# Optimization experiments

Measured on AMD Instinct MI355X. Metric: run time of the kernel, lower is better.

The kernel has to match this reference:

```python
import jax, jax.numpy as jnp
import numpy as np

B, N, NS, D, H = 32, 4096, 16, 512, 8
DH = D // H          # dims_per_head = 64
DFF = 4 * D          # ff_mlp hidden
SCALE = DH ** -0.5
EPS = 1e-8           # slot-attention renorm eps
LN_EPS = 1e-5        # torch LayerNorm default
ITERS = 3


def layer_norm(x, g, b):
    mu = jnp.mean(x, axis=-1, keepdims=True)
    var = jnp.mean((x - mu) ** 2, axis=-1, keepdims=True)
    return (x - mu) * jax.lax.rsqrt(var + LN_EPS) * g + b


def setup_inputs() -> dict:
    key = jax.random.key(0)
    ks = jax.random.split(key, 8)
    s = 0.02
    return {
        "inputs": jax.random.normal(ks[0], (B, N, D), jnp.float32),
        "conditioning": jax.random.normal(ks[1], (B, NS, D), jnp.float32),
        # norm_input
        "ln_in_g": jnp.ones((D,), jnp.float32),
        "ln_in_b": jnp.zeros((D,), jnp.float32),
        # projections (no bias: use_projection_bias=False)
        "Wk": jax.random.normal(ks[2], (D, D), jnp.float32) * s,
        "Wv": jax.random.normal(ks[3], (D, D), jnp.float32) * s,
        "Wq": jax.random.normal(ks[4], (D, D), jnp.float32) * s,
        "Wo": jax.random.normal(ks[5], (D, D), jnp.float32) * s,
        # norm_slots / norm_slots_ff_mlp
        "ln_s_g": jnp.ones((D,), jnp.float32),
        "ln_s_b": jnp.zeros((D,), jnp.float32),
        "ln_f_g": jnp.ones((D,), jnp.float32),
        "ln_f_b": jnp.zeros((D,), jnp.float32),
        # ff_mlp: Linear(D,4D) -> ReLU -> Linear(4D,D)
        "W1": jax.random.normal(ks[6], (D, DFF), jnp.float32) * s,
        "b1": jnp.zeros((DFF,), jnp.float32),
        "W2": jax.random.normal(ks[7], (DFF, D), jnp.float32) * s,
        "b2": jnp.zeros((D,), jnp.float32),
    }


def reference(inputs, conditioning, ln_in_g, ln_in_b, Wk, Wv, Wq, Wo,
              ln_s_g, ln_s_b, ln_f_g, ln_f_b, W1, b1, W2, b2):
    b = inputs.shape[0]
    x = layer_norm(inputs, ln_in_g, ln_in_b)                 # [b, n, D]
    k = (x @ Wk.T).reshape(b, N, H, DH)                      # [b, n, h, dh]
    v = (x @ Wv.T).reshape(b, N, H, DH)

    slots = conditioning
    attn_mean = None
    for _ in range(ITERS):
        slots_prev = slots
        s = layer_norm(slots, ln_s_g, ln_s_b)
        q = (s @ Wq.T).reshape(b, NS, H, DH)                 # [b, ns, h, dh]
        dots = jnp.einsum("bihd,bjhd->bihj", q, k) * SCALE   # [b, ns, h, n]
        # softmax over flattened (slots, heads) axis, per input location j
        attn = jax.nn.softmax(dots.reshape(b, NS * H, N), axis=1)
        attn = attn.reshape(b, NS, H, N)
        attn_before = attn
        attn = attn + EPS
        attn = attn / jnp.sum(attn, axis=-1, keepdims=True)  # renorm over j
        updates = jnp.einsum("bjhd,bihj->bihd", v, attn)     # [b, ns, h, dh]
        updates = updates.reshape(b, NS, D)
        slots = updates @ Wo.T + slots_prev                  # to_o + residual
        slots_prev_ff = slots
        s2 = layer_norm(slots, ln_f_g, ln_f_b)
        s2 = jax.nn.relu(s2 @ W1 + b1) @ W2 + b2             # ff_mlp
        slots = s2 + slots_prev_ff
        attn_mean = jnp.mean(attn_before, axis=2)            # [b, ns, n]
    return slots, attn_mean
```

## Files before the change

### kernel.cpp

```cpp
#include <hip/hip_runtime.h>
#include <cstdint>
#include <cstddef>

typedef __attribute__((ext_vector_type(8))) short short8;
typedef __attribute__((ext_vector_type(4))) short short4v;
typedef __attribute__((ext_vector_type(8))) __bf16 bf16x8;
typedef __attribute__((ext_vector_type(4))) float f32x4;
typedef unsigned short u16;

static constexpr int Bb = 32, Nn = 4096, NSs = 16, Dd = 512, Hh = 8, DFF = 2048;
static constexpr float SCALE = 0.125f;
static constexpr float EPSR  = 1e-8f;
static constexpr float LN_EPS = 1e-5f;

__device__ __forceinline__ u16 f2b(float x) {
  union { float f; uint32_t u; } a; a.f = x;
  uint32_t r = a.u + 0x7fffu + ((a.u >> 16) & 1u);
  return (u16)(r >> 16);
}

__device__ __forceinline__ f32x4 mfma16(short8 a, short8 b, f32x4 c) {
  return __builtin_amdgcn_mfma_f32_16x16x32_bf16(
      __builtin_bit_cast(bf16x8, a), __builtin_bit_cast(bf16x8, b), c, 0, 0, 0);
}

__device__ __forceinline__ void gload16(const u16* g, u16* l) {
  __builtin_amdgcn_global_load_lds(
      (const __attribute__((address_space(1))) void*)g,
      (__attribute__((address_space(3))) void*)l, 16, 0, 0);
}


__global__ __launch_bounds__(256) void ln_rows(const float* __restrict__ src,
    const float* __restrict__ g, const float* __restrict__ bt,
    u16* __restrict__ dst, int R) {
  int row = blockIdx.x * 4 + (threadIdx.x >> 6);
  if (row >= R) return;
  int lane = threadIdx.x & 63;
  const float* p = src + (size_t)row * Dd + lane * 8;
  float4 u0 = *(const float4*)p;
  float4 u1 = *(const float4*)(p + 4);
  float x[8] = {u0.x,u0.y,u0.z,u0.w,u1.x,u1.y,u1.z,u1.w};
  float s = 0.f, s2 = 0.f;
#pragma unroll
  for (int e = 0; e < 8; ++e) { s += x[e]; s2 += x[e]*x[e]; }
#pragma unroll
  for (int m = 1; m < 64; m <<= 1) { s += __shfl_xor(s, m); s2 += __shfl_xor(s2, m); }
  float mean = s * (1.f/512.f);
  float var  = s2 * (1.f/512.f) - mean*mean;
  float rstd = rsqrtf(var + LN_EPS);
  union { u16 o[8]; short8 v; } ou;
#pragma unroll
  for (int e = 0; e < 8; ++e)
    ou.o[e] = f2b((x[e]-mean)*rstd*g[lane*8+e] + bt[lane*8+e]);
  *(short8*)(dst + (size_t)row * Dd + lane * 8) = ou.v;
}

__global__ __launch_bounds__(256, 2) void gemm_kv(const u16* __restrict__ A,
    const u16* __restrict__ Bk, const u16* __restrict__ Bv,
    u16* __restrict__ Ck, u16* __restrict__ CvT) {
  __shared__ u16 lA[2][128*32];
  __shared__ u16 lK[2][128*32];
  __shared__ u16 lV[2][128*32];
  const int tid = threadIdx.x, lane = tid & 63, wid = tid >> 6;
  const int wr = wid >> 1, wc = wid & 1;
  const int n  = blockIdx.y * 4 + blockIdx.x;
  const int orig = (n & 7) * 512 + (n >> 3);
  const int bm = (orig >> 2) * 128, bn = (orig & 3) * 128;
  const size_t BN = (size_t)Bb * Nn;
  f32x4 ak[4][4] = {};
  f32x4 av[4][4] = {};
  const int srow = wid*16 + (lane >> 2);
  const int scol = ((lane & 3) ^ ((lane >> 3) & 3)) * 8;
  const u16* Ap = A  + (size_t)(bm + srow) * Dd + scol;
  const u16* Kp = Bk + (size_t)(bn + srow) * Dd + scol;
  const u16* Vp = Bv + (size_t)(bn + srow) * Dd + scol;
  const int ldb = wid * 512;
  const int li = lane & 15, lk = lane >> 4;
  const int csw = (lk ^ ((li >> 1) & 3)) * 8;
  gload16(Ap, &lA[0][ldb]);
  gload16(Ap + (size_t)64*Dd, &lA[0][ldb + 2048]);
  gload16(Kp, &lK[0][ldb]);
  gload16(Kp + (size_t)64*Dd, &lK[0][ldb + 2048]);
  gload16(Vp, &lV[0][ldb]);
  gload16(Vp + (size_t)64*Dd, &lV[0][ldb + 2048]);
  int cur = 0;
  for (int t = 0; t < 16; ++t) {
    __syncthreads();
    const int nx = cur ^ 1;
    if (t < 15) {
      const int k0 = (t + 1) * 32;
      gload16(Ap + k0, &lA[nx][ldb]);
      gload16(Ap + (size_t)64*Dd + k0, &lA[nx][ldb + 2048]);
      gload16(Kp + k0, &lK[nx][ldb]);
      gload16(Kp + (size_t)64*Dd + k0, &lK[nx][ldb + 2048]);
      gload16(Vp + k0, &lV[nx][ldb]);
      gload16(Vp + (size_t)64*Dd + k0, &lV[nx][ldb + 2048]);
    }
    short8 af[4], kf[4], vf[4];
#pragma unroll
    for (int m = 0; m < 4; ++m)
      af[m] = *(const short8*)&lA[cur][(wr*64 + m*16 + li)*32 + csw];
#pragma unroll
    for (int nn2 = 0; nn2 < 4; ++nn2) {
      kf[nn2] = *(const short8*)&lK[cur][(wc*64 + nn2*16 + li)*32 + csw];
      vf[nn2] = *(const short8*)&lV[cur][(wc*64 + nn2*16 + li)*32 + csw];
    }
#pragma unroll
    for (int m = 0; m < 4; ++m)
#pragma unroll
      for (int nn2 = 0; nn2 < 4; ++nn2) {
        ak[m][nn2] = mfma16(af[m], kf[nn2], ak[m][nn2]);
        av[m][nn2] = mfma16(af[m], vf[nn2], av[m][nn2]);
      }
    cur = nx;
  }
  const int lr = lk * 4;
#pragma unroll
  for (int m = 0; m < 4; ++m)
#pragma unroll
    for (int nn2 = 0; nn2 < 4; ++nn2) {
      int row = bm + wr*64 + m*16 + lr;
      int col = bn + wc*64 + nn2*16 + li;
      f32x4 vk = ak[m][nn2];
#pragma unroll
      for (int r = 0; r < 4; ++r)
        Ck[(size_t)(row + r) * Dd + col] = f2b(vk[r]);
      f32x4 vv = av[m][nn2];
      union { u16 o[4]; short4v v4; } ou;
#pragma unroll
      for (int r = 0; r < 4; ++r) ou.o[r] = f2b(vv[r]);
      *(short4v*)&CvT[(size_t)col * BN + row] = ou.v4;
    }
}

template<int EP>
__global__ __launch_bounds__(256) void gemm64(const u16* __restrict__ A,
    const u16* __restrict__ Bw, void* __restrict__ Cp,
    const float* __restrict__ bias, const float* __restrict__ res,
    int N, int K) {
  __shared__ u16 lA[2][64*32];
  __shared__ u16 lB[2][64*32];
  const int tid = threadIdx.x, lane = tid & 63, wid = tid >> 6;
  const int wr = wid >> 1, wc = wid & 1;
  const int bm = blockIdx.y * 64, bn = blockIdx.x * 64;
  f32x4 acc[2][2] = {};
  const int srow = wid*16 + (lane >> 2);
  const int scol = ((lane & 3) ^ ((lane >> 3) & 3)) * 8;
  const u16* Ap = A + (size_t)(bm + srow) * K + scol;
  const u16* Bp = Bw + (size_t)(bn + srow) * K + scol;
  const int ldb = wid * 512;
  const int li = lane & 15, lk = lane >> 4;
  const int csw = (lk ^ ((li >> 1) & 3)) * 8;
  const int nsteps = K >> 5;
  gload16(Ap, &lA[0][ldb]);
  gload16(Bp, &lB[0][ldb]);
  int cur = 0;
  for (int t = 0; t < nsteps; ++t) {
    __syncthreads();
    const int nx = cur ^ 1;
    if (t + 1 < nsteps) {
      const int k0 = (t + 1) * 32;
      gload16(Ap + k0, &lA[nx][ldb]);
      gload16(Bp + k0, &lB[nx][ldb]);
    }
    short8 af[2], bf[2];
#pragma unroll
    for (int m = 0; m < 2; ++m)
      af[m] = *(const short8*)&lA[cur][(wr*32 + m*16 + li)*32 + csw];
#pragma unroll
    for (int nn2 = 0; nn2 < 2; ++nn2)
      bf[nn2] = *(const short8*)&lB[cur][(wc*32 + nn2*16 + li)*32 + csw];
#pragma unroll
    for (int m = 0; m < 2; ++m)
#pragma unroll
      for (int nn2 = 0; nn2 < 2; ++nn2)
        acc[m][nn2] = mfma16(af[m], bf[nn2], acc[m][nn2]);
    cur = nx;
  }
  const int lr = lk * 4;
#pragma unroll
  for (int m = 0; m < 2; ++m)
#pragma unroll
    for (int nn2 = 0; nn2 < 2; ++nn2) {
      int row = bm + wr*32 + m*16 + lr;
      int col = bn + wc*32 + nn2*16 + li;
      f32x4 v = acc[m][nn2];
#pragma unroll
      for (int r = 0; r < 4; ++r) {
        size_t off = (size_t)(row + r) * N + col;
        float x = v[r];
        if constexpr (EP == 0) ((u16*)Cp)[off] = f2b(x);
        else if constexpr (EP == 1) ((float*)Cp)[off] = x + res[off];
        else if constexpr (EP == 2) { x += bias[col]; ((u16*)Cp)[off] = f2b(x > 0.f ? x : 0.f); }
        else ((float*)Cp)[off] = x + bias[col] + res[off];
      }
    }
}

__global__ __launch_bounds__(256) void attn_a(const u16* __restrict__ q,
    const u16* __restrict__ kk, u16* __restrict__ attnb,
    float* __restrict__ rowsum, float* __restrict__ attn_mean) {
  const int jt = blockIdx.x, b = blockIdx.y;
  const int tid = threadIdx.x, lane = tid & 63, wid = tid >> 6;
  __shared__ float sc[64][129];
  __shared__ float red[4][64];
  const int li = lane & 15, lk = lane >> 4;
#pragma unroll
  for (int hh = 0; hh < 2; ++hh) {
    const int h = wid * 2 + hh;
    const u16* qb = q + (((size_t)b*16 + li)*8 + h)*64 + lk*8;
    short8 a0 = *(const short8*)qb;
    short8 a1 = *(const short8*)(qb + 32);
#pragma unroll
    for (int n = 0; n < 4; ++n) {
      const u16* kb = kk + ((size_t)b*Nn + jt*64 + n*16 + li)*Dd + h*64 + lk*8;
      f32x4 acc = {};
      acc = mfma16(a0, *(const short8*)kb, acc);
      acc = mfma16(a1, *(const short8*)(kb + 32), acc);
#pragma unroll
      for (int r = 0; r < 4; ++r)
        sc[n*16 + li][(lk*4 + r)*8 + h] = acc[r] * SCALE;
    }
  }
  __syncthreads();
  const int jl = tid & 63, qt = tid >> 6;
  float mx = -1e30f;
#pragma unroll
  for (int e = 0; e < 32; ++e) mx = fmaxf(mx, sc[jl][qt*32 + e]);
  red[qt][jl] = mx;
  __syncthreads();
  float M = fmaxf(fmaxf(red[0][jl], red[1][jl]), fmaxf(red[2][jl], red[3][jl]));
  __syncthreads();
  float s = 0.f;
#pragma unroll
  for (int e = 0; e < 32; ++e) {
    float ev = __expf(sc[jl][qt*32 + e] - M);
    sc[jl][qt*32 + e] = ev; s += ev;
  }
  red[qt][jl] = s;
  __syncthreads();
  float S = red[0][jl] + red[1][jl] + red[2][jl] + red[3][jl];
  float inv = 1.f / S;
#pragma unroll
  for (int e = 0; e < 32; ++e)
    sc[jl][qt*32 + e] = sc[jl][qt*32 + e] * inv + EPSR;
  __syncthreads();
  if (tid < 128) {
    float rs = 0.f;
    for (int j2 = 0; j2 < 64; ++j2) rs += sc[j2][tid];
    atomicAdd(&rowsum[b*128 + tid], rs);
  }
#pragma unroll
  for (int e = 0; e < 32; ++e) {
    int r = qt*32 + e;
    attnb[((size_t)b*128 + r)*Nn + jt*64 + jl] = f2b(sc[jl][r]);
  }
  if (attn_mean != nullptr && tid < 64) {
    for (int i = 0; i < 16; ++i) {
      float sm = 0.f;
#pragma unroll
      for (int h = 0; h < 8; ++h) sm += sc[tid][i*8 + h];
      attn_mean[((size_t)b*16 + i)*Nn + jt*64 + tid] = sm * 0.125f - EPSR;
    }
  }
}

__global__ __launch_bounds__(256) void attn_b(const u16* __restrict__ attnb,
    const u16* __restrict__ vT, const float* __restrict__ rowsum,
    u16* __restrict__ upd) {
  const int h = blockIdx.x, b = blockIdx.y;
  const int lane = threadIdx.x & 63, wid = threadIdx.x >> 6;
  const int li = lane & 15, lk = lane >> 4;
  const size_t BN = (size_t)Bb * Nn;
  const u16* Ap = attnb + ((size_t)b*128 + li*8 + h)*Nn + lk*8;
  const u16* Bp = vT + (size_t)(h*64 + wid*16 + li)*BN + (size_t)b*Nn + lk*8;
  f32x4 acc[4] = {};
  for (int k0 = 0; k0 < Nn; k0 += 128) {
#pragma unroll
    for (int e = 0; e < 4; ++e)
      acc[e] = mfma16(*(const short8*)(Ap + k0 + e*32),
                      *(const short8*)(Bp + k0 + e*32), acc[e]);
  }
#pragma unroll
  for (int r = 0; r < 4; ++r) {
    int i = lk*4 + r;
    float t = acc[0][r] + acc[1][r] + acc[2][r] + acc[3][r];
    float rs = rowsum[b*128 + i*8 + h];
    upd[((size_t)b*16 + i)*Dd + h*64 + wid*16 + li] = f2b(t / rs);
  }
}

__global__ void cvt_w(const float* __restrict__ s, u16* __restrict__ d, int n) {
  int i = blockIdx.x*256 + threadIdx.x;
  if (i < n) d[i] = f2b(s[i]);
}
__global__ __launch_bounds__(256) void tr_cvt(const float* __restrict__ s,
    u16* __restrict__ d, int R, int C) {
  __shared__ u16 t[32][33];
  const int c0 = blockIdx.x*32, r0 = blockIdx.y*32;
  const int tr = threadIdx.x >> 3, tc4 = (threadIdx.x & 7)*4;
  float4 v = *(const float4*)&s[(size_t)(r0+tr)*C + c0 + tc4];
  t[tr][tc4+0] = f2b(v.x); t[tr][tc4+1] = f2b(v.y);
  t[tr][tc4+2] = f2b(v.z); t[tr][tc4+3] = f2b(v.w);
  __syncthreads();
  const int oc = threadIdx.x >> 3, or4 = (threadIdx.x & 7)*4;
  union { u16 o[4]; short4v v4; } ou;
#pragma unroll
  for (int e = 0; e < 4; ++e) ou.o[e] = t[or4+e][oc];
  *(short4v*)&d[(size_t)(c0+oc)*R + r0 + or4] = ou.v4;
}
__global__ void copy_f32v4(const float* __restrict__ s, float* __restrict__ d, int n4) {
  int i = blockIdx.x*256 + threadIdx.x;
  if (i < n4) ((float4*)d)[i] = ((const float4*)s)[i];
}

extern "C" void kernel_launch(void* const* d_in, const int* in_sizes, int n_in,
                              void* d_out, int out_size, void* d_ws, size_t ws_size,
                              hipStream_t stream) {
  (void)in_sizes; (void)n_in; (void)out_size; (void)ws_size;
  const float* inputs  = (const float*)d_in[0];
  const float* cond    = (const float*)d_in[1];
  const float* ln_in_g = (const float*)d_in[2];
  const float* ln_in_b = (const float*)d_in[3];
  const float* Wk = (const float*)d_in[4];
  const float* Wv = (const float*)d_in[5];
  const float* Wq = (const float*)d_in[6];
  const float* Wo = (const float*)d_in[7];
  const float* ln_s_g = (const float*)d_in[8];
  const float* ln_s_b = (const float*)d_in[9];
  const float* ln_f_g = (const float*)d_in[10];
  const float* ln_f_b = (const float*)d_in[11];
  const float* W1 = (const float*)d_in[12];
  const float* b1 = (const float*)d_in[13];
  const float* W2 = (const float*)d_in[14];
  const float* b2 = (const float*)d_in[15];
  float* out_slots = (float*)d_out;
  float* out_amean = (float*)d_out + (size_t)Bb*NSs*Dd;

  char* w = (char*)d_ws;
  auto alloc = [&](size_t bytes) {
    char* p = w; w += (bytes + 255) & ~(size_t)255; return p;
  };
  u16*  xn    = (u16*)alloc((size_t)Bb*Nn*Dd*2);
  u16*  kbuf  = (u16*)alloc((size_t)Bb*Nn*Dd*2);
  u16*  vT    = (u16*)alloc((size_t)Bb*Nn*Dd*2);
  u16*  attnb = (u16*)alloc((size_t)Bb*128*Nn*2);
  float* slots = (float*)alloc((size_t)Bb*NSs*Dd*4);
  u16*  qb    = (u16*)alloc((size_t)Bb*NSs*Dd*2);
  u16*  snb   = (u16*)alloc((size_t)Bb*NSs*Dd*2);
  u16*  s2nb  = (u16*)alloc((size_t)Bb*NSs*Dd*2);
  u16*  h1b   = (u16*)alloc((size_t)Bb*NSs*DFF*2);
  u16*  updb  = (u16*)alloc((size_t)Bb*NSs*Dd*2);
  float* rowsum = (float*)alloc((size_t)Bb*128*3*4);
  u16*  wkb = (u16*)alloc(262144*2);
  u16*  wvb = (u16*)alloc(262144*2);
  u16*  wqb = (u16*)alloc(262144*2);
  u16*  wob = (u16*)alloc(262144*2);
  u16*  w1t = (u16*)alloc((size_t)1048576*2);
  u16*  w2t = (u16*)alloc((size_t)1048576*2);

  cvt_w<<<1024, 256, 0, stream>>>(Wk, wkb, 262144);
  cvt_w<<<1024, 256, 0, stream>>>(Wv, wvb, 262144);
  cvt_w<<<1024, 256, 0, stream>>>(Wq, wqb, 262144);
  cvt_w<<<1024, 256, 0, stream>>>(Wo, wob, 262144);
  tr_cvt<<<dim3(64, 16), 256, 0, stream>>>(W1, w1t, 512, 2048);
  tr_cvt<<<dim3(16, 64), 256, 0, stream>>>(W2, w2t, 2048, 512);
  copy_f32v4<<<256, 256, 0, stream>>>(cond, slots, 65536);
  hipMemsetAsync(rowsum, 0, (size_t)Bb*128*3*4, stream);
  ln_rows<<<Bb*Nn/4, 256, 0, stream>>>(inputs, ln_in_g, ln_in_b, xn, Bb*Nn);
  gemm_kv<<<dim3(4, Bb*Nn/128), 256, 0, stream>>>(xn, wkb, wvb, kbuf, vT);

  for (int it = 0; it < 3; ++it) {
    float* rs = rowsum + (size_t)it * Bb * 128;
    ln_rows<<<128, 256, 0, stream>>>(slots, ln_s_g, ln_s_b, snb, Bb*NSs);
    gemm64<0><<<dim3(8, 8), 256, 0, stream>>>(snb, wqb, qb, nullptr, nullptr, 512, 512);
    attn_a<<<dim3(Nn/64, Bb), 256, 0, stream>>>(qb, kbuf, attnb, rs,
                                                it == 2 ? out_amean : nullptr);
    attn_b<<<dim3(Hh, Bb), 256, 0, stream>>>(attnb, vT, rs, updb);
    gemm64<1><<<dim3(8, 8), 256, 0, stream>>>(updb, wob, slots, nullptr, slots, 512, 512);
    ln_rows<<<128, 256, 0, stream>>>(slots, ln_f_g, ln_f_b, s2nb, Bb*NSs);
    gemm64<2><<<dim3(32, 8), 256, 0, stream>>>(s2nb, w1t, h1b, b1, nullptr, 2048, 512);
    gemm64<3><<<dim3(8, 8), 256, 0, stream>>>(h1b, w2t, slots, b2, slots, 512, 2048);
  }
  copy_f32v4<<<256, 256, 0, stream>>>(slots, out_slots, 65536);
}
```

Baseline: 720.5 us.

## Fold Wk and Wv into per-iteration query/update projections instead of materializing K and V

Removes the large K/V projection GEMM over all B*N tokens. Each iteration instead computes q' = q·Wk per head, takes scores directly against the normalized inputs, aggregates attention-weighted xn, and then applies Wv to the small result. This trades one large GEMM for a larger inner dimension in the attention kernels (512 instead of 64 per head) plus a transpose of xn. It also adds several new small kernels (qp_k, upd_k) that use scalar FMA loops, and split-j partial sums written to a float buffer.

```diff
diff --git a/kernel.cpp b/kernel.cpp
--- a/kernel.cpp
+++ b/kernel.cpp
@@ -18,6 +18,9 @@
   uint32_t r = a.u + 0x7fffu + ((a.u >> 16) & 1u);
   return (u16)(r >> 16);
 }
+__device__ __forceinline__ float b2f(u16 x) {
+  union { uint32_t u; float f; } a; a.u = ((uint32_t)x) << 16; return a.f;
+}
 
 __device__ __forceinline__ f32x4 mfma16(short8 a, short8 b, f32x4 c) {
   return __builtin_amdgcn_mfma_f32_16x16x32_bf16(
@@ -29,7 +32,6 @@
       (const __attribute__((address_space(1))) void*)g,
       (__attribute__((address_space(3))) void*)l, 16, 0, 0);
 }
-
 
 __global__ __launch_bounds__(256) void ln_rows(const float* __restrict__ src,
     const float* __restrict__ g, const float* __restrict__ bt,
@@ -54,84 +56,6 @@
   for (int e = 0; e < 8; ++e)
     ou.o[e] = f2b((x[e]-mean)*rstd*g[lane*8+e] + bt[lane*8+e]);
   *(short8*)(dst + (size_t)row * Dd + lane * 8) = ou.v;
-}
-
-__global__ __launch_bounds__(256, 2) void gemm_kv(const u16* __restrict__ A,
-    const u16* __restrict__ Bk, const u16* __restrict__ Bv,
-    u16* __restrict__ Ck, u16* __restrict__ CvT) {
-  __shared__ u16 lA[2][128*32];
-  __shared__ u16 lK[2][128*32];
-  __shared__ u16 lV[2][128*32];
-  const int tid = threadIdx.x, lane = tid & 63, wid = tid >> 6;
-  const int wr = wid >> 1, wc = wid & 1;
-  const int n  = blockIdx.y * 4 + blockIdx.x;
-  const int orig = (n & 7) * 512 + (n >> 3);
-  const int bm = (orig >> 2) * 128, bn = (orig & 3) * 128;
-  const size_t BN = (size_t)Bb * Nn;
-  f32x4 ak[4][4] = {};
-  f32x4 av[4][4] = {};
-  const int srow = wid*16 + (lane >> 2);
-  const int scol = ((lane & 3) ^ ((lane >> 3) & 3)) * 8;
-  const u16* Ap = A  + (size_t)(bm + srow) * Dd + scol;
-  const u16* Kp = Bk + (size_t)(bn + srow) * Dd + scol;
-  const u16* Vp = Bv + (size_t)(bn + srow) * Dd + scol;
-  const int ldb = wid * 512;
-  const int li = lane & 15, lk = lane >> 4;
-  const int csw = (lk ^ ((li >> 1) & 3)) * 8;
-  gload16(Ap, &lA[0][ldb]);
-  gload16(Ap + (size_t)64*Dd, &lA[0][ldb + 2048]);
-  gload16(Kp, &lK[0][ldb]);
-  gload16(Kp + (size_t)64*Dd, &lK[0][ldb + 2048]);
-  gload16(Vp, &lV[0][ldb]);
-  gload16(Vp + (size_t)64*Dd, &lV[0][ldb + 2048]);
-  int cur = 0;
-  for (int t = 0; t < 16; ++t) {
-    __syncthreads();
-    const int nx = cur ^ 1;
-    if (t < 15) {
-      const int k0 = (t + 1) * 32;
-      gload16(Ap + k0, &lA[nx][ldb]);
-      gload16(Ap + (size_t)64*Dd + k0, &lA[nx][ldb + 2048]);
-      gload16(Kp + k0, &lK[nx][ldb]);
-      gload16(Kp + (size_t)64*Dd + k0, &lK[nx][ldb + 2048]);
-      gload16(Vp + k0, &lV[nx][ldb]);
-      gload16(Vp + (size_t)64*Dd + k0, &lV[nx][ldb + 2048]);
-    }
-    short8 af[4], kf[4], vf[4];
-#pragma unroll
-    for (int m = 0; m < 4; ++m)
-      af[m] = *(const short8*)&lA[cur][(wr*64 + m*16 + li)*32 + csw];
-#pragma unroll
-    for (int nn2 = 0; nn2 < 4; ++nn2) {
-      kf[nn2] = *(const short8*)&lK[cur][(wc*64 + nn2*16 + li)*32 + csw];
-      vf[nn2] = *(const short8*)&lV[cur][(wc*64 + nn2*16 + li)*32 + csw];
-    }
-#pragma unroll
-    for (int m = 0; m < 4; ++m)
-#pragma unroll
-      for (int nn2 = 0; nn2 < 4; ++nn2) {
-        ak[m][nn2] = mfma16(af[m], kf[nn2], ak[m][nn2]);
-        av[m][nn2] = mfma16(af[m], vf[nn2], av[m][nn2]);
-      }
-    cur = nx;
-  }
-  const int lr = lk * 4;
-#pragma unroll
-  for (int m = 0; m < 4; ++m)
-#pragma unroll
-    for (int nn2 = 0; nn2 < 4; ++nn2) {
-      int row = bm + wr*64 + m*16 + lr;
-      int col = bn + wc*64 + nn2*16 + li;
-      f32x4 vk = ak[m][nn2];
-#pragma unroll
-      for (int r = 0; r < 4; ++r)
-        Ck[(size_t)(row + r) * Dd + col] = f2b(vk[r]);
-      f32x4 vv = av[m][nn2];
-      union { u16 o[4]; short4v v4; } ou;
-#pragma unroll
-      for (int r = 0; r < 4; ++r) ou.o[r] = f2b(vv[r]);
-      *(short4v*)&CvT[(size_t)col * BN + row] = ou.v4;
-    }
 }
 
 template<int EP>
@@ -198,36 +122,73 @@
     }
 }
 
-__global__ __launch_bounds__(256) void attn_a(const u16* __restrict__ q,
-    const u16* __restrict__ kk, u16* __restrict__ attnb,
+__global__ __launch_bounds__(256) void qp_k(const u16* __restrict__ qb,
+    const u16* __restrict__ wkT, u16* __restrict__ qpb) {
+  int idx = blockIdx.x * 256 + threadIdx.x;
+  int e = idx & 511, row = idx >> 9;
+  int h = row & 7, bi = row >> 3;
+  const u16* qr = qb + (size_t)bi * 512 + h * 64;
+  const u16* wr = wkT + (size_t)e * 512 + h * 64;
+  float a = 0.f;
+#pragma unroll
+  for (int d = 0; d < 64; d += 8) {
+    short8 qv = *(const short8*)(qr + d);
+    short8 wv = *(const short8*)(wr + d);
+#pragma unroll
+    for (int t = 0; t < 8; ++t) a += b2f((u16)qv[t]) * b2f((u16)wv[t]);
+  }
+  qpb[idx] = f2b(a);
+}
+
+__global__ __launch_bounds__(256) void attn_a2(const u16* __restrict__ qp,
+    const u16* __restrict__ xn, u16* __restrict__ attnb,
     float* __restrict__ rowsum, float* __restrict__ attn_mean) {
   const int jt = blockIdx.x, b = blockIdx.y;
   const int tid = threadIdx.x, lane = tid & 63, wid = tid >> 6;
-  __shared__ float sc[64][129];
+  __shared__ u16 lxn[64 * 512];
   __shared__ float red[4][64];
+  float (*sc)[129] = (float(*)[129])lxn;
+  {
+    const u16* base = xn + ((size_t)b * Nn + jt * 64) * Dd;
+#pragma unroll
+    for (int r2 = 0; r2 < 16; ++r2) {
+      int j = r2 * 4 + wid;
+      gload16(base + (size_t)j * Dd + ((lane ^ (j & 7)) * 8), &lxn[j * 512]);
+    }
+  }
+  __syncthreads();
   const int li = lane & 15, lk = lane >> 4;
-#pragma unroll
-  for (int hh = 0; hh < 2; ++hh) {
-    const int h = wid * 2 + hh;
-    const u16* qb = q + (((size_t)b*16 + li)*8 + h)*64 + lk*8;
-    short8 a0 = *(const short8*)qb;
-    short8 a1 = *(const short8*)(qb + 32);
+  f32x4 acc[2][4] = {};
+  const u16* qbase = qp + ((size_t)b * 128 + wid * 32) * Dd;
+  for (int k = 0; k < 16; ++k) {
+    short8 af[2], bf[4];
+#pragma unroll
+    for (int m = 0; m < 2; ++m)
+      af[m] = *(const short8*)(qbase + (size_t)(m * 16 + li) * Dd + k * 32 + lk * 8);
 #pragma unroll
     for (int n = 0; n < 4; ++n) {
-      const u16* kb = kk + ((size_t)b*Nn + jt*64 + n*16 + li)*Dd + h*64 + lk*8;
-      f32x4 acc = {};
-      acc = mfma16(a0, *(const short8*)kb, acc);
-      acc = mfma16(a1, *(const short8*)(kb + 32), acc);
+      int j = n * 16 + li;
+      bf[n] = *(const short8*)&lxn[j * 512 + (((k * 4 + lk) ^ (li & 7)) * 8)];
+    }
+#pragma unroll
+    for (int m = 0; m < 2; ++m)
+#pragma unroll
+      for (int n = 0; n < 4; ++n)
+        acc[m][n] = mfma16(af[m], bf[n], acc[m][n]);
+  }
+  __syncthreads();
+#pragma unroll
+  for (int m = 0; m < 2; ++m)
+#pragma unroll
+    for (int n = 0; n < 4; ++n)
 #pragma unroll
       for (int r = 0; r < 4; ++r)
-        sc[n*16 + li][(lk*4 + r)*8 + h] = acc[r] * SCALE;
-    }
-  }
+        sc[n * 16 + li][wid * 32 + m * 16 + lk * 4 + r] = acc[m][n][r] * SCALE;
   __syncthreads();
   const int jl = tid & 63, qt = tid >> 6;
   float mx = -1e30f;
 #pragma unroll
-  for (int e = 0; e < 32; ++e) mx = fmaxf(mx, sc[jl][qt*32 + e]);
+  for (int e = 0; e < 32; ++e) mx = fmaxf(mx, sc[jl][qt * 32 + e]);
   red[qt][jl] = mx;
   __syncthreads();
   float M = fmaxf(fmaxf(red[0][jl], red[1][jl]), fmaxf(red[2][jl], red[3][jl]));
@@ -235,8 +196,8 @@
   float s = 0.f;
 #pragma unroll
   for (int e = 0; e < 32; ++e) {
-    float ev = __expf(sc[jl][qt*32 + e] - M);
-    sc[jl][qt*32 + e] = ev; s += ev;
+    float ev = __expf(sc[jl][qt * 32 + e] - M);
+    sc[jl][qt * 32 + e] = ev; s += ev;
   }
   red[qt][jl] = s;
   __syncthreads();
@@ -244,50 +205,82 @@
   float inv = 1.f / S;
 #pragma unroll
   for (int e = 0; e < 32; ++e)
-    sc[jl][qt*32 + e] = sc[jl][qt*32 + e] * inv + EPSR;
+    sc[jl][qt * 32 + e] = sc[jl][qt * 32 + e] * inv + EPSR;
   __syncthreads();
   if (tid < 128) {
     float rs = 0.f;
     for (int j2 = 0; j2 < 64; ++j2) rs += sc[j2][tid];
-    atomicAdd(&rowsum[b*128 + tid], rs);
+    atomicAdd(&rowsum[b * 128 + tid], rs);
   }
 #pragma unroll
   for (int e = 0; e < 32; ++e) {
-    int r = qt*32 + e;
-    attnb[((size_t)b*128 + r)*Nn + jt*64 + jl] = f2b(sc[jl][r]);
+    int r = qt * 32 + e;
+    attnb[((size_t)b * 128 + r) * Nn + jt * 64 + jl] = f2b(sc[jl][r]);
   }
   if (attn_mean != nullptr && tid < 64) {
     for (int i = 0; i < 16; ++i) {
       float sm = 0.f;
 #pragma unroll
-      for (int h = 0; h < 8; ++h) sm += sc[tid][i*8 + h];
-      attn_mean[((size_t)b*16 + i)*Nn + jt*64 + tid] = sm * 0.125f - EPSR;
-    }
-  }
-}
-
-__global__ __launch_bounds__(256) void attn_b(const u16* __restrict__ attnb,
-    const u16* __restrict__ vT, const float* __restrict__ rowsum,
-    u16* __restrict__ upd) {
-  const int h = blockIdx.x, b = blockIdx.y;
+      for (int h = 0; h < 8; ++h) sm += sc[tid][i * 8 + h];
+      attn_mean[((size_t)b * 16 + i) * Nn + jt * 64 + tid] = sm * 0.125f - EPSR;
+    }
+  }
+}
+
+__global__ __launch_bounds__(256) void attn_b2(const u16* __restrict__ attnb,
+    const u16* __restrict__ xnT, float* __restrict__ Tpart) {
+  const int et = blockIdx.x, jh = blockIdx.y, b = blockIdx.z;
   const int lane = threadIdx.x & 63, wid = threadIdx.x >> 6;
   const int li = lane & 15, lk = lane >> 4;
   const size_t BN = (size_t)Bb * Nn;
-  const u16* Ap = attnb + ((size_t)b*128 + li*8 + h)*Nn + lk*8;
-  const u16* Bp = vT + (size_t)(h*64 + wid*16 + li)*BN + (size_t)b*Nn + lk*8;
-  f32x4 acc[4] = {};
-  for (int k0 = 0; k0 < Nn; k0 += 128) {
-#pragma unroll
-    for (int e = 0; e < 4; ++e)
-      acc[e] = mfma16(*(const short8*)(Ap + k0 + e*32),
-                      *(const short8*)(Bp + k0 + e*32), acc[e]);
-  }
-#pragma unroll
-  for (int r = 0; r < 4; ++r) {
-    int i = lk*4 + r;
-    float t = acc[0][r] + acc[1][r] + acc[2][r] + acc[3][r];
-    float rs = rowsum[b*128 + i*8 + h];
-    upd[((size_t)b*16 + i)*Dd + h*64 + wid*16 + li] = f2b(t / rs);
+  const int j0 = jh * 2048;
+  const u16* Ap = attnb + ((size_t)b * 128 + wid * 32 + li) * Nn + j0 + lk * 8;
+  const u16* Bp = xnT + (size_t)(et * 64 + li) * BN + (size_t)b * Nn + j0 + lk * 8;
+  f32x4 acc[2][4] = {};
+  for (int k0 = 0; k0 < 2048; k0 += 32) {
+    short8 af[2], bf[4];
+#pragma unroll
+    for (int m = 0; m < 2; ++m) af[m] = *(const short8*)(Ap + (size_t)m * 16 * Nn + k0);
+#pragma unroll
+    for (int n = 0; n < 4; ++n) bf[n] = *(const short8*)(Bp + (size_t)n * 16 * BN + k0);
+#pragma unroll
+    for (int m = 0; m < 2; ++m)
+#pragma unroll
+      for (int n = 0; n < 4; ++n)
+        acc[m][n] = mfma16(af[m], bf[n], acc[m][n]);
+  }
+  float* Tout = Tpart + ((size_t)jh * Bb + b) * 128 * 512;
+#pragma unroll
+  for (int m = 0; m < 2; ++m)
+#pragma unroll
+    for (int n = 0; n < 4; ++n)
+#pragma unroll
+      for (int r = 0; r < 4; ++r)
+        Tout[(size_t)(wid * 32 + m * 16 + lk * 4 + r) * 512 + et * 64 + n * 16 + li]
+            = acc[m][n][r];
+}
+
+__global__ __launch_bounds__(256) void upd_k(const float* __restrict__ Tpart,
+    const u16* __restrict__ wvT, const float* __restrict__ rs,
+    u16* __restrict__ updb) {
+  const int bi = blockIdx.x;
+  const int b = bi >> 4, i = bi & 15;
+  const int tid = threadIdx.x;
+  __shared__ float lT[8][512];
+  const float* T0 = Tpart + ((size_t)b * 128 + i * 8) * 512;
+  const float* T1 = T0 + (size_t)Bb * 128 * 512;
+  for (int t = tid; t < 4096; t += 256)
+    lT[t >> 9][t & 511] = T0[t] + T1[t];
+  __syncthreads();
+#pragma unroll
+  for (int half = 0; half < 2; ++half) {
+    int o = half * 256 + tid;
+    int h = o >> 6;
+    float a = 0.f;
+    for (int e = 0; e < 512; ++e)
+      a += lT[h][e] * b2f(wvT[(size_t)e * 512 + o]);
+    float r = rs[b * 128 + i * 8 + h];
+    updb[(size_t)bi * 512 + o] = f2b(a / r);
   }
 }
 
@@ -303,6 +296,21 @@
   float4 v = *(const float4*)&s[(size_t)(r0+tr)*C + c0 + tc4];
   t[tr][tc4+0] = f2b(v.x); t[tr][tc4+1] = f2b(v.y);
   t[tr][tc4+2] = f2b(v.z); t[tr][tc4+3] = f2b(v.w);
+  __syncthreads();
+  const int oc = threadIdx.x >> 3, or4 = (threadIdx.x & 7)*4;
+  union { u16 o[4]; short4v v4; } ou;
+#pragma unroll
+  for (int e = 0; e < 4; ++e) ou.o[e] = t[or4+e][oc];
+  *(short4v*)&d[(size_t)(c0+oc)*R + r0 + or4] = ou.v4;
+}
+__global__ __launch_bounds__(256) void tr16(const u16* __restrict__ s,
+    u16* __restrict__ d, int R, int C) {
+  __shared__ u16 t[32][33];
+  const int c0 = blockIdx.x*32, r0 = blockIdx.y*32;
+  const int tr = threadIdx.x >> 3, tc4 = (threadIdx.x & 7)*4;
+  short4v v = *(const short4v*)&s[(size_t)(r0+tr)*C + c0 + tc4];
+  t[tr][tc4+0] = (u16)v[0]; t[tr][tc4+1] = (u16)v[1];
+  t[tr][tc4+2] = (u16)v[2]; t[tr][tc4+3] = (u16)v[3];
   __syncthreads();
   const int oc = threadIdx.x >> 3, or4 = (threadIdx.x & 7)*4;
   union { u16 o[4]; short4v v4; } ou;
@@ -343,41 +351,44 @@
     char* p = w; w += (bytes + 255) & ~(size_t)255; return p;
   };
   u16*  xn    = (u16*)alloc((size_t)Bb*Nn*Dd*2);
-  u16*  kbuf  = (u16*)alloc((size_t)Bb*Nn*Dd*2);
-  u16*  vT    = (u16*)alloc((size_t)Bb*Nn*Dd*2);
+  u16*  xnT   = (u16*)alloc((size_t)Bb*Nn*Dd*2);
   u16*  attnb = (u16*)alloc((size_t)Bb*128*Nn*2);
+  float* Tpart = (float*)alloc((size_t)2*Bb*128*512*4);
   float* slots = (float*)alloc((size_t)Bb*NSs*Dd*4);
   u16*  qb    = (u16*)alloc((size_t)Bb*NSs*Dd*2);
+  u16*  qpb   = (u16*)alloc((size_t)Bb*128*Dd*2);
   u16*  snb   = (u16*)alloc((size_t)Bb*NSs*Dd*2);
   u16*  s2nb  = (u16*)alloc((size_t)Bb*NSs*Dd*2);
   u16*  h1b   = (u16*)alloc((size_t)Bb*NSs*DFF*2);
   u16*  updb  = (u16*)alloc((size_t)Bb*NSs*Dd*2);
   float* rowsum = (float*)alloc((size_t)Bb*128*3*4);
-  u16*  wkb = (u16*)alloc(262144*2);
-  u16*  wvb = (u16*)alloc(262144*2);
   u16*  wqb = (u16*)alloc(262144*2);
   u16*  wob = (u16*)alloc(262144*2);
+  u16*  wkT = (u16*)alloc(262144*2);
+  u16*  wvT = (u16*)alloc(262144*2);
   u16*  w1t = (u16*)alloc((size_t)1048576*2);
   u16*  w2t = (u16*)alloc((size_t)1048576*2);
 
-  cvt_w<<<1024, 256, 0, stream>>>(Wk, wkb, 262144);
-  cvt_w<<<1024, 256, 0, stream>>>(Wv, wvb, 262144);
   cvt_w<<<1024, 256, 0, stream>>>(Wq, wqb, 262144);
   cvt_w<<<1024, 256, 0, stream>>>(Wo, wob, 262144);
+  tr_cvt<<<dim3(16, 16), 256, 0, stream>>>(Wk, wkT, 512, 512);
+  tr_cvt<<<dim3(16, 16), 256, 0, stream>>>(Wv, wvT, 512, 512);
   tr_cvt<<<dim3(64, 16), 256, 0, stream>>>(W1, w1t, 512, 2048);
   tr_cvt<<<dim3(16, 64), 256, 0, stream>>>(W2, w2t, 2048, 512);
   copy_f32v4<<<256, 256, 0, stream>>>(cond, slots, 65536);
   hipMemsetAsync(rowsum, 0, (size_t)Bb*128*3*4, stream);
   ln_rows<<<Bb*Nn/4, 256, 0, stream>>>(inputs, ln_in_g, ln_in_b, xn, Bb*Nn);
-  gemm_kv<<<dim3(4, Bb*Nn/128), 256, 0, stream>>>(xn, wkb, wvb, kbuf, vT);
+  tr16<<<dim3(16, Bb*Nn/32), 256, 0, stream>>>(xn, xnT, Bb*Nn, 512);
 
   for (int it = 0; it < 3; ++it) {
-    float* rs = rowsum + (size_t)it * Bb * 128;
+    float* rsp = rowsum + (size_t)it * Bb * 128;
     ln_rows<<<128, 256, 0, stream>>>(slots, ln_s_g, ln_s_b, snb, Bb*NSs);
     gemm64<0><<<dim3(8, 8), 256, 0, stream>>>(snb, wqb, qb, nullptr, nullptr, 512, 512);
-    attn_a<<<dim3(Nn/64, Bb), 256, 0, stream>>>(qb, kbuf, attnb, rs,
-                                                it == 2 ? out_amean : nullptr);
-    attn_b<<<dim3(Hh, Bb), 256, 0, stream>>>(attnb, vT, rs, updb);
+    qp_k<<<8192, 256, 0, stream>>>(qb, wkT, qpb);
+    attn_a2<<<dim3(Nn/64, Bb), 256, 0, stream>>>(qpb, xn, attnb, rsp,
+                                                 it == 2 ? out_amean : nullptr);
+    attn_b2<<<dim3(8, 2, Bb), 256, 0, stream>>>(attnb, xnT, Tpart);
+    upd_k<<<Bb*NSs, 256, 0, stream>>>(Tpart, wvT, rsp, updb);
     gemm64<1><<<dim3(8, 8), 256, 0, stream>>>(updb, wob, slots, nullptr, slots, 512, 512);
     ln_rows<<<128, 256, 0, stream>>>(slots, ln_f_g, ln_f_b, s2nb, Bb*NSs);
     gemm64<2><<<dim3(32, 8), 256, 0, stream>>>(s2nb, w1t, h1b, b1, nullptr, 2048, 512);
```

New measurement: 1.128 ms. 1.57x slower.

## Split attn_b over sequence chunks and restage gemm_kv with 64-wide K tiles

Applied to the files above, without the earlier changes.

attn_b now splits the 4096-long reduction into four 1024 chunks, which launches 4x more blocks. The chunks write fp32 partial sums, and a new upd_c kernel reduces them and divides by rowsum. The goal is to fill more CUs in the small-grid attention-value product, at the cost of one extra launch and a small partial buffer. gemm_kv separately moves from double-buffered 32-wide K tiles to single-buffered 64-wide tiles with an XOR swizzle and two barriers per step. This halves the loop trip count but removes the overlap between loads and MFMA.

```diff
diff --git a/kernel.cpp b/kernel.cpp
--- a/kernel.cpp
+++ b/kernel.cpp
@@ -29,7 +29,6 @@
       (const __attribute__((address_space(1))) void*)g,
       (__attribute__((address_space(3))) void*)l, 16, 0, 0);
 }
-
 
 __global__ __launch_bounds__(256) void ln_rows(const float* __restrict__ src,
     const float* __restrict__ g, const float* __restrict__ bt,
@@ -59,9 +58,9 @@
 __global__ __launch_bounds__(256, 2) void gemm_kv(const u16* __restrict__ A,
     const u16* __restrict__ Bk, const u16* __restrict__ Bv,
     u16* __restrict__ Ck, u16* __restrict__ CvT) {
-  __shared__ u16 lA[2][128*32];
-  __shared__ u16 lK[2][128*32];
-  __shared__ u16 lV[2][128*32];
+  __shared__ u16 lA[128*64];
+  __shared__ u16 lK[128*64];
+  __shared__ u16 lV[128*64];
   const int tid = threadIdx.x, lane = tid & 63, wid = tid >> 6;
   const int wr = wid >> 1, wc = wid & 1;
   const int n  = blockIdx.y * 4 + blockIdx.x;
@@ -70,50 +69,41 @@
   const size_t BN = (size_t)Bb * Nn;
   f32x4 ak[4][4] = {};
   f32x4 av[4][4] = {};
-  const int srow = wid*16 + (lane >> 2);
-  const int scol = ((lane & 3) ^ ((lane >> 3) & 3)) * 8;
-  const u16* Ap = A  + (size_t)(bm + srow) * Dd + scol;
-  const u16* Kp = Bk + (size_t)(bn + srow) * Dd + scol;
-  const u16* Vp = Bv + (size_t)(bn + srow) * Dd + scol;
-  const int ldb = wid * 512;
+  const int sr = lane >> 3;
+  const int ss = ((lane & 7) ^ (sr & 7)) * 8;
   const int li = lane & 15, lk = lane >> 4;
-  const int csw = (lk ^ ((li >> 1) & 3)) * 8;
-  gload16(Ap, &lA[0][ldb]);
-  gload16(Ap + (size_t)64*Dd, &lA[0][ldb + 2048]);
-  gload16(Kp, &lK[0][ldb]);
-  gload16(Kp + (size_t)64*Dd, &lK[0][ldb + 2048]);
-  gload16(Vp, &lV[0][ldb]);
-  gload16(Vp + (size_t)64*Dd, &lV[0][ldb + 2048]);
-  int cur = 0;
-  for (int t = 0; t < 16; ++t) {
+  const int sx = (li & 7) * 8;
+  for (int t = 0; t < 8; ++t) {
+    const int k0 = t * 64;
     __syncthreads();
-    const int nx = cur ^ 1;
-    if (t < 15) {
-      const int k0 = (t + 1) * 32;
-      gload16(Ap + k0, &lA[nx][ldb]);
-      gload16(Ap + (size_t)64*Dd + k0, &lA[nx][ldb + 2048]);
-      gload16(Kp + k0, &lK[nx][ldb]);
-      gload16(Kp + (size_t)64*Dd + k0, &lK[nx][ldb + 2048]);
-      gload16(Vp + k0, &lV[nx][ldb]);
-      gload16(Vp + (size_t)64*Dd + k0, &lV[nx][ldb + 2048]);
-    }
-    short8 af[4], kf[4], vf[4];
-#pragma unroll
-    for (int m = 0; m < 4; ++m)
-      af[m] = *(const short8*)&lA[cur][(wr*64 + m*16 + li)*32 + csw];
-#pragma unroll
-    for (int nn2 = 0; nn2 < 4; ++nn2) {
-      kf[nn2] = *(const short8*)&lK[cur][(wc*64 + nn2*16 + li)*32 + csw];
-      vf[nn2] = *(const short8*)&lV[cur][(wc*64 + nn2*16 + li)*32 + csw];
-    }
-#pragma unroll
-    for (int m = 0; m < 4; ++m)
+#pragma unroll
+    for (int gi = 0; gi < 4; ++gi) {
+      const int rb = wid * 32 + gi * 8;
+      gload16(A  + (size_t)(bm + rb + sr) * Dd + k0 + ss, &lA[rb * 64]);
+      gload16(Bk + (size_t)(bn + rb + sr) * Dd + k0 + ss, &lK[rb * 64]);
+      gload16(Bv + (size_t)(bn + rb + sr) * Dd + k0 + ss, &lV[rb * 64]);
+    }
+    __syncthreads();
+#pragma unroll
+    for (int kk = 0; kk < 2; ++kk) {
+      const int cs = ((kk * 4 + lk) * 8) ^ sx;
+      short8 af[4], kf[4], vf[4];
+#pragma unroll
+      for (int m = 0; m < 4; ++m)
+        af[m] = *(const short8*)&lA[(wr*64 + m*16 + li)*64 + cs];
 #pragma unroll
       for (int nn2 = 0; nn2 < 4; ++nn2) {
-        ak[m][nn2] = mfma16(af[m], kf[nn2], ak[m][nn2]);
-        av[m][nn2] = mfma16(af[m], vf[nn2], av[m][nn2]);
+        kf[nn2] = *(const short8*)&lK[(wc*64 + nn2*16 + li)*64 + cs];
+        vf[nn2] = *(const short8*)&lV[(wc*64 + nn2*16 + li)*64 + cs];
       }
-    cur = nx;
+#pragma unroll
+      for (int m = 0; m < 4; ++m)
+#pragma unroll
+        for (int nn2 = 0; nn2 < 4; ++nn2) {
+          ak[m][nn2] = mfma16(af[m], kf[nn2], ak[m][nn2]);
+          av[m][nn2] = mfma16(af[m], vf[nn2], av[m][nn2]);
+        }
+    }
   }
   const int lr = lk * 4;
 #pragma unroll
@@ -267,28 +257,41 @@
 }
 
 __global__ __launch_bounds__(256) void attn_b(const u16* __restrict__ attnb,
-    const u16* __restrict__ vT, const float* __restrict__ rowsum,
-    u16* __restrict__ upd) {
-  const int h = blockIdx.x, b = blockIdx.y;
+    const u16* __restrict__ vT, float* __restrict__ Tpart) {
+  const int h = blockIdx.x, js = blockIdx.y, b = blockIdx.z;
   const int lane = threadIdx.x & 63, wid = threadIdx.x >> 6;
   const int li = lane & 15, lk = lane >> 4;
   const size_t BN = (size_t)Bb * Nn;
-  const u16* Ap = attnb + ((size_t)b*128 + li*8 + h)*Nn + lk*8;
-  const u16* Bp = vT + (size_t)(h*64 + wid*16 + li)*BN + (size_t)b*Nn + lk*8;
+  const int j0 = js * 1024;
+  const u16* Ap = attnb + ((size_t)b*128 + li*8 + h)*Nn + j0 + lk*8;
+  const u16* Bp = vT + (size_t)(h*64 + wid*16 + li)*BN + (size_t)b*Nn + j0 + lk*8;
   f32x4 acc[4] = {};
-  for (int k0 = 0; k0 < Nn; k0 += 128) {
+  for (int k0 = 0; k0 < 1024; k0 += 128) {
 #pragma unroll
     for (int e = 0; e < 4; ++e)
       acc[e] = mfma16(*(const short8*)(Ap + k0 + e*32),
                       *(const short8*)(Bp + k0 + e*32), acc[e]);
   }
+  float* Tout = Tpart + ((((size_t)js * Bb + b) * 8 + h) * 16) * 64;
 #pragma unroll
   for (int r = 0; r < 4; ++r) {
     int i = lk*4 + r;
     float t = acc[0][r] + acc[1][r] + acc[2][r] + acc[3][r];
-    float rs = rowsum[b*128 + i*8 + h];
-    upd[((size_t)b*16 + i)*Dd + h*64 + wid*16 + li] = f2b(t / rs);
-  }
+    Tout[(size_t)i * 64 + wid*16 + li] = t;
+  }
+}
+
+__global__ void upd_c(const float* __restrict__ Tpart,
+    const float* __restrict__ rs, u16* __restrict__ updb) {
+  int idx = blockIdx.x * 256 + threadIdx.x;
+  int o = idx & 511, bi = idx >> 9;
+  int b = bi >> 4, i = bi & 15;
+  int h = o >> 6, d = o & 63;
+  size_t base = (((size_t)b * 8 + h) * 16 + i) * 64 + d;
+  const size_t stride = (size_t)Bb * 8 * 16 * 64;
+  float t = Tpart[base] + Tpart[base + stride]
+          + Tpart[base + 2*stride] + Tpart[base + 3*stride];
+  updb[idx] = f2b(t / rs[b * 128 + i * 8 + h]);
 }
 
 __global__ void cvt_w(const float* __restrict__ s, u16* __restrict__ d, int n) {
@@ -346,6 +349,7 @@
   u16*  kbuf  = (u16*)alloc((size_t)Bb*Nn*Dd*2);
   u16*  vT    = (u16*)alloc((size_t)Bb*Nn*Dd*2);
   u16*  attnb = (u16*)alloc((size_t)Bb*128*Nn*2);
+  float* Tpart = (float*)alloc((size_t)4*Bb*8*16*64*4);
   float* slots = (float*)alloc((size_t)Bb*NSs*Dd*4);
   u16*  qb    = (u16*)alloc((size_t)Bb*NSs*Dd*2);
   u16*  snb   = (u16*)alloc((size_t)Bb*NSs*Dd*2);
@@ -367,17 +371,18 @@
   tr_cvt<<<dim3(64, 16), 256, 0, stream>>>(W1, w1t, 512, 2048);
   tr_cvt<<<dim3(16, 64), 256, 0, stream>>>(W2, w2t, 2048, 512);
   copy_f32v4<<<256, 256, 0, stream>>>(cond, slots, 65536);
-  hipMemsetAsync(rowsum, 0, (size_t)Bb*128*3*4, stream);
+  (void)hipMemsetAsync(rowsum, 0, (size_t)Bb*128*3*4, stream);
   ln_rows<<<Bb*Nn/4, 256, 0, stream>>>(inputs, ln_in_g, ln_in_b, xn, Bb*Nn);
   gemm_kv<<<dim3(4, Bb*Nn/128), 256, 0, stream>>>(xn, wkb, wvb, kbuf, vT);
 
   for (int it = 0; it < 3; ++it) {
-    float* rs = rowsum + (size_t)it * Bb * 128;
+    float* rsp = rowsum + (size_t)it * Bb * 128;
     ln_rows<<<128, 256, 0, stream>>>(slots, ln_s_g, ln_s_b, snb, Bb*NSs);
     gemm64<0><<<dim3(8, 8), 256, 0, stream>>>(snb, wqb, qb, nullptr, nullptr, 512, 512);
-    attn_a<<<dim3(Nn/64, Bb), 256, 0, stream>>>(qb, kbuf, attnb, rs,
+    attn_a<<<dim3(Nn/64, Bb), 256, 0, stream>>>(qb, kbuf, attnb, rsp,
                                                 it == 2 ? out_amean : nullptr);
-    attn_b<<<dim3(Hh, Bb), 256, 0, stream>>>(attnb, vT, rs, updb);
+    attn_b<<<dim3(Hh, 4, Bb), 256, 0, stream>>>(attnb, vT, Tpart);
+    upd_c<<<1024, 256, 0, stream>>>(Tpart, rsp, updb);
     gemm64<1><<<dim3(8, 8), 256, 0, stream>>>(updb, wob, slots, nullptr, slots, 512, 512);
     ln_rows<<<128, 256, 0, stream>>>(slots, ln_f_g, ln_f_b, s2nb, Bb*NSs);
     gemm64<2><<<dim3(32, 8), 256, 0, stream>>>(s2nb, w1t, h1b, b1, nullptr, 2048, 512);
```

After: 706.3 us. 1.02x faster.
